# Kernel tuning notes

Measured on AMD Instinct MI355X. Metric: run time of the kernel, lower is better.

## Reference

```python
import jax, jax.numpy as jnp
import numpy as np

NUM_GROUPS = 512
GROUP_SIZE = 32
GROUP_RADIUS = 0.2
K_ORIGINAL = 5 * GROUP_SIZE  # ball_query oversampling factor from the source


def setup_inputs() -> dict:
    key = jax.random.key(0)
    k1, k2 = jax.random.split(key)
    B, N, C = 8, 16384, 4
    points = jax.random.normal(k1, (B, N, C), dtype=jnp.float32)
    # valid lengths in [N//2, N) so the lengths-masking path is exercised
    lengths = (N // 2 + jax.random.randint(k2, (B,), 0, N // 2)).astype(jnp.int32)
    return {"points": points, "lengths": lengths}


def _sample_farthest_points(xyz, lengths, K):
    # xyz: (B,N,3) float, lengths: (B,) int -> centers (B,K,3)
    B, N, _ = xyz.shape
    n_idx = jnp.arange(N)

    def per_batch(pts, length):
        valid = n_idx < length

        def step(carry, _):
            mindist, cur = carry
            d = jnp.sum((pts - pts[cur]) ** 2, axis=-1)  # (N,)
            mindist = jnp.where(valid, jnp.minimum(mindist, d), -jnp.inf)
            nxt = jnp.argmax(mindist).astype(jnp.int32)
            return (mindist, nxt), cur

        mindist0 = jnp.where(valid, jnp.inf, -jnp.inf)
        # deterministic start at index 0 (source uses random_start_point=True)
        (_, _), sel = jax.lax.scan(step, (mindist0, jnp.int32(0)), None, length=K)
        return pts[sel]

    return jax.vmap(per_batch)(xyz, lengths)


def _ball_query(centers, xyz, lengths, K, radius):
    # returns first-K (by point index, matching pytorch3d ball_query) indices
    # within radius; -1 padding. centers (B,G,3), xyz (B,N,3) -> idx (B,G,K)
    B, G, _ = centers.shape
    N = xyz.shape[1]
    d2 = jnp.sum((centers[:, :, None, :] - xyz[:, None, :, :]) ** 2, axis=-1)  # (B,G,N)
    valid = (jnp.arange(N) < lengths[:, None])[:, None, :]  # (B,1,N)
    mask = (d2 < radius * radius) & valid
    # score N-n > 0 iff in ball; top_k picks smallest indices first (in order)
    score = jnp.where(mask, N - jnp.arange(N, dtype=jnp.int32), jnp.int32(-1))
    vals, _ = jax.lax.top_k(score, K)
    return jnp.where(vals > 0, N - vals, -1)  # (B,G,K)


def _select_topk_by_energy(points, idx, K_new):
    # points (B,N,C), idx (B,G,K_orig) with -1 invalid -> (B,G,K_new)
    B, G, _ = idx.shape
    N = points.shape[1]
    invalid = idx == -1
    idxc = jnp.maximum(idx, 0)
    energies = jnp.broadcast_to(points[:, None, :, 3], (B, G, N))
    e = jnp.take_along_axis(energies, idxc, axis=2)  # (B,G,K_orig)
    e = jnp.where(invalid, -jnp.inf, e)
    top_e, top_i = jax.lax.top_k(e, K_new)
    topk_idx = jnp.take_along_axis(idx, top_i, axis=2)
    return jnp.where(top_e == -jnp.inf, -1, topk_idx)


def _masked_gather(points, idx):
    # points (B,N,C), idx (B,G,K); -1 -> gathered value 0.0 (pytorch3d semantics)
    B, G, K = idx.shape
    C = points.shape[-1]
    valid = idx >= 0
    flat = jnp.maximum(idx, 0).reshape(B, G * K)
    g = jnp.take_along_axis(points, flat[:, :, None], axis=1).reshape(B, G, K, C)
    return jnp.where(valid[..., None], g, 0.0)


def _forward(points, lengths):
    xyz = points[:, :, :3]
    centers = _sample_farthest_points(xyz, lengths, NUM_GROUPS)  # (B,G,3)
    idx = _ball_query(centers, xyz, lengths, K_ORIGINAL, GROUP_RADIUS)
    idx = _select_topk_by_energy(points, idx, GROUP_SIZE)  # (B,G,K)
    # fill_empty_indices: replace -1 with first index of the group
    first = idx[:, :, :1]
    idx = jnp.where(idx == -1, first, idx)
    groups = _masked_gather(points, idx)  # (B,G,K,C)
    groups = jnp.concatenate(
        [groups[..., :3] - centers[:, :, None, :], groups[..., 3:]], axis=-1
    )
    groups = groups / GROUP_RADIUS
    return groups, centers


def reference(points, lengths):
    return _forward(points, lengths)
```

## Files before the change

### kernel.cpp

```cpp
#include <hip/hip_runtime.h>

constexpr int B_ = 8;
constexpr int N_ = 16384;
constexpr int NG = 512;
constexpr int GS = 32;
constexpr int KORIG = 160;
constexpr int TPB = 512;
constexpr int PPT = 32;
#define R2 0.04f
#define RADIUS 0.2f

__device__ __forceinline__ unsigned f32_ord(float f) {
  unsigned u = __float_as_uint(f);
  return (u & 0x80000000u) ? ~u : (u | 0x80000000u);
}

template <int CTRL>
__device__ __forceinline__ float dpp_fmax(float v) {
  int o = __builtin_amdgcn_update_dpp(0, __float_as_int(v), CTRL, 0xF, 0xF, true);
  return fmaxf(v, __int_as_float(o));
}
__device__ __forceinline__ float wave_fmax(float v) {
  v = dpp_fmax<0xB1>(v);
  v = dpp_fmax<0x4E>(v);
  v = dpp_fmax<0x141>(v);
  v = dpp_fmax<0x140>(v);
  v = fmaxf(v, __int_as_float(__builtin_amdgcn_ds_swizzle(__float_as_int(v), 0x401F)));
  v = fmaxf(v, __shfl_xor(v, 32, 64));
  return v;
}
__device__ __forceinline__ float group8_fmax(float v) {
  v = dpp_fmax<0xB1>(v);
  v = dpp_fmax<0x4E>(v);
  v = dpp_fmax<0x141>(v);
  return v;
}

__global__ __launch_bounds__(512) void fps_kernel(const float4* __restrict__ p4,
                                                  const int* __restrict__ lengths,
                                                  float* __restrict__ centers) {
#pragma clang fp contract(off)
  const int b = blockIdx.x;
  const int t = threadIdx.x;
  const int lane = t & 63;
  const int wid = t >> 6;
  const int len = lengths[b];
  const float4* bp = p4 + (size_t)b * N_;

  __shared__ unsigned long long pub[2][8];

  float x[PPT], y[PPT], z[PPT], m[PPT];
#pragma unroll
  for (int j = 0; j < PPT; ++j) {
    const int i = t * PPT + j;
    float4 p = bp[i];
    x[j] = p.x; y[j] = p.y; z[j] = p.z;
    m[j] = (i < len) ? __builtin_inff() : -__builtin_inff();
  }

  float4 c0 = bp[0];
  float cx = c0.x, cy = c0.y, cz = c0.z;
  if (t == 0) {
    size_t o = (size_t)b * NG * 3;
    centers[o] = cx; centers[o + 1] = cy; centers[o + 2] = cz;
  }

  for (int k = 0; k < NG - 1; ++k) {
#pragma unroll
    for (int j = 0; j < PPT; ++j) {
      float dx = x[j] - cx;
      float dy = y[j] - cy;
      float dz = z[j] - cz;
      float d = dx * dx + dy * dy + dz * dz;
      m[j] = fminf(m[j], d);
    }
    float u0 = fmaxf(m[0], m[1]),   u1 = fmaxf(m[2], m[3]);
    float u2 = fmaxf(m[4], m[5]),   u3 = fmaxf(m[6], m[7]);
    float u4 = fmaxf(m[8], m[9]),   u5 = fmaxf(m[10], m[11]);
    float u6 = fmaxf(m[12], m[13]), u7 = fmaxf(m[14], m[15]);
    float u8 = fmaxf(m[16], m[17]), u9 = fmaxf(m[18], m[19]);
    float uA = fmaxf(m[20], m[21]), uB = fmaxf(m[22], m[23]);
    float uC = fmaxf(m[24], m[25]), uD = fmaxf(m[26], m[27]);
    float uE = fmaxf(m[28], m[29]), uF = fmaxf(m[30], m[31]);
    float v0 = fmaxf(u0, u1), v1 = fmaxf(u2, u3), v2 = fmaxf(u4, u5), v3 = fmaxf(u6, u7);
    float v4 = fmaxf(u8, u9), v5 = fmaxf(uA, uB), v6 = fmaxf(uC, uD), v7 = fmaxf(uE, uF);
    float w0 = fmaxf(v0, v1), w1 = fmaxf(v2, v3), w2 = fmaxf(v4, v5), w3 = fmaxf(v6, v7);
    const float sm = fmaxf(fmaxf(w0, w1), fmaxf(w2, w3));
    int bj = 31;
#pragma unroll
    for (int j = 30; j >= 0; --j) bj = (m[j] == sm) ? j : bj;

    const float wmax = wave_fmax(sm);
    const unsigned long long att = __ballot(sm == wmax);
    const int wl = __ffsll((unsigned long long)att) - 1;
    if (lane == wl) {
      pub[k & 1][wid] = ((unsigned long long)__float_as_uint(wmax) << 32) |
                        (unsigned)(t * PPT + bj);
    }
    __syncthreads();

    const unsigned long long pv = pub[k & 1][lane & 7];
    const float pw = __uint_as_float((unsigned)(pv >> 32));
    const int pi = (int)(unsigned)(pv & 0xFFFFFFFFull);
    const float4 pc = bp[pi];
    const float kmax = group8_fmax(pw);
    const unsigned long long bal = __ballot(pw == kmax);
    const int grp = lane & 56;
    const int winw = grp + (__ffsll((bal >> grp) & 0xFFull) - 1);
    cx = __shfl(pc.x, winw, 64);
    cy = __shfl(pc.y, winw, 64);
    cz = __shfl(pc.z, winw, 64);

    if (t == 0) {
      size_t o = ((size_t)b * NG + (k + 1)) * 3;
      centers[o] = cx; centers[o + 1] = cy; centers[o + 2] = cz;
    }
  }
}

__global__ __launch_bounds__(64) void group_kernel(const float4* __restrict__ p4,
                                                   const int* __restrict__ lengths,
                                                   const float* __restrict__ centers,
                                                   float4* __restrict__ outg) {
#pragma clang fp contract(off)
  const int gid = blockIdx.x;
  const int b = gid >> 9;
  const int lane = threadIdx.x;
  const int len = lengths[b];
  const float4* bp = p4 + (size_t)b * N_;
  const float cx = centers[(size_t)gid * 3 + 0];
  const float cy = centers[(size_t)gid * 3 + 1];
  const float cz = centers[(size_t)gid * 3 + 2];

  __shared__ int cand[KORIG];
  int M = 0;
  for (int cb = 0; cb < N_ && M < KORIG; cb += 256) {
#pragma unroll
    for (int q = 0; q < 4; ++q) {
      const int i = cb + q * 64 + lane;
      float4 p = bp[i];
      float dx = p.x - cx;
      float dy = p.y - cy;
      float dz = p.z - cz;
      float d2 = dx * dx + dy * dy + dz * dz;
      const bool pred = (i < len) && (d2 < R2);
      unsigned long long mb = __ballot(pred);
      if (pred) {
        int pos = M + (int)__popcll(mb & ((1ull << lane) - 1ull));
        if (pos < KORIG) cand[pos] = i;
      }
      M += (int)__popcll(mb);
    }
  }
  if (M > KORIG) M = KORIG;
  __syncthreads();

  const unsigned long long SENT = ~0ull;
  unsigned long long key0 = SENT, key1 = SENT, key2 = SENT;
  {
    int c0 = lane, c1 = lane + 64, c2 = lane + 128;
    if (c0 < M) { int i = cand[c0]; key0 = ((unsigned long long)(~f32_ord(bp[i].w)) << 32) | (unsigned)i; }
    if (c1 < M) { int i = cand[c1]; key1 = ((unsigned long long)(~f32_ord(bp[i].w)) << 32) | (unsigned)i; }
    if (c2 < M) { int i = cand[c2]; key2 = ((unsigned long long)(~f32_ord(bp[i].w)) << 32) | (unsigned)i; }
  }

  int mysel = -1;
  for (int j = 0; j < GS; ++j) {
    unsigned long long kmin = key0 < key1 ? key0 : key1;
    if (key2 < kmin) kmin = key2;
#pragma unroll
    for (int off = 32; off > 0; off >>= 1) {
      unsigned long long o = __shfl_xor(kmin, off, 64);
      if (o < kmin) kmin = o;
    }
    if (kmin == SENT) break;
    if (lane == j) mysel = (int)(unsigned)kmin;
    if (key0 == kmin) key0 = SENT;
    if (key1 == kmin) key1 = SENT;
    if (key2 == kmin) key2 = SENT;
  }

  const int first = __shfl(mysel, 0, 64);
  if (lane < GS) {
    int idx = (mysel < 0) ? first : mysel;
    float4 o;
    if (idx >= 0) {
      float4 p = bp[idx];
      o.x = (p.x - cx) / RADIUS;
      o.y = (p.y - cy) / RADIUS;
      o.z = (p.z - cz) / RADIUS;
      o.w = p.w / RADIUS;
    } else {
      o.x = (0.0f - cx) / RADIUS;
      o.y = (0.0f - cy) / RADIUS;
      o.z = (0.0f - cz) / RADIUS;
      o.w = 0.0f;
    }
    outg[(size_t)gid * GS + lane] = o;
  }
}

extern "C" void kernel_launch(void* const* d_in, const int* in_sizes, int n_in,
                              void* d_out, int out_size, void* d_ws, size_t ws_size,
                              hipStream_t stream) {
  const float4* pts = (const float4*)d_in[0];
  const int* lengths = (const int*)d_in[1];
  float* out = (float*)d_out;
  float* centers = out + (size_t)B_ * NG * GS * 4;
  float4* groups = (float4*)out;

  fps_kernel<<<B_, TPB, 0, stream>>>(pts, lengths, centers);
  group_kernel<<<B_ * NG, 64, 0, stream>>>(pts, lengths, centers, groups);
}
```

Before: 1.003 ms.

## Resolve FPS argmax in winning wave from registers instead of global reload

Result: slower. 1.204 ms (+20.1%).

```diff
diff --git a/kernel.cpp b/kernel.cpp
--- a/kernel.cpp
+++ b/kernel.cpp
@@ -36,9 +36,9 @@
   return v;
 }
 
-__global__ __launch_bounds__(512) void fps_kernel(const float4* __restrict__ p4,
-                                                  const int* __restrict__ lengths,
-                                                  float* __restrict__ centers) {
+__global__ __launch_bounds__(512, 2) void fps_kernel(const float4* __restrict__ p4,
+                                                     const int* __restrict__ lengths,
+                                                     float* __restrict__ centers) {
 #pragma clang fp contract(off)
   const int b = blockIdx.x;
   const int t = threadIdx.x;
@@ -47,7 +47,8 @@
   const int len = lengths[b];
   const float4* bp = p4 + (size_t)b * N_;
 
-  __shared__ unsigned long long pub[2][8];
+  __shared__ float pubf[8];
+  __shared__ float4 cpub;
 
   float x[PPT], y[PPT], z[PPT], m[PPT];
 #pragma unroll
@@ -86,31 +87,36 @@
     float v4 = fmaxf(u8, u9), v5 = fmaxf(uA, uB), v6 = fmaxf(uC, uD), v7 = fmaxf(uE, uF);
     float w0 = fmaxf(v0, v1), w1 = fmaxf(v2, v3), w2 = fmaxf(v4, v5), w3 = fmaxf(v6, v7);
     const float sm = fmaxf(fmaxf(w0, w1), fmaxf(w2, w3));
-    int bj = 31;
-#pragma unroll
-    for (int j = 30; j >= 0; --j) bj = (m[j] == sm) ? j : bj;
 
     const float wmax = wave_fmax(sm);
-    const unsigned long long att = __ballot(sm == wmax);
-    const int wl = __ffsll((unsigned long long)att) - 1;
-    if (lane == wl) {
-      pub[k & 1][wid] = ((unsigned long long)__float_as_uint(wmax) << 32) |
-                        (unsigned)(t * PPT + bj);
-    }
+    if (lane == 0) pubf[wid] = wmax;
     __syncthreads();
 
-    const unsigned long long pv = pub[k & 1][lane & 7];
-    const float pw = __uint_as_float((unsigned)(pv >> 32));
-    const int pi = (int)(unsigned)(pv & 0xFFFFFFFFull);
-    const float4 pc = bp[pi];
+    const float pw = pubf[lane & 7];
     const float kmax = group8_fmax(pw);
     const unsigned long long bal = __ballot(pw == kmax);
     const int grp = lane & 56;
-    const int winw = grp + (__ffsll((bal >> grp) & 0xFFull) - 1);
-    cx = __shfl(pc.x, winw, 64);
-    cy = __shfl(pc.y, winw, 64);
-    cz = __shfl(pc.z, winw, 64);
-
+    const int ww = __ffsll((bal >> grp) & 0xFFull) - 1;
+
+    if (wid == ww) {
+      float gx = x[0], gy = y[0], gz = z[0];
+      bool fnd = (m[0] == kmax);
+#pragma unroll
+      for (int j = 1; j < PPT; ++j) {
+        const bool sel = (m[j] == kmax) && !fnd;
+        gx = sel ? x[j] : gx;
+        gy = sel ? y[j] : gy;
+        gz = sel ? z[j] : gz;
+        fnd = fnd || sel;
+      }
+      const unsigned long long mb = __ballot(fnd);
+      const int wl = __ffsll(mb) - 1;
+      if (lane == wl) cpub = make_float4(gx, gy, gz, 0.0f);
+    }
+    __syncthreads();
+
+    const float4 c = cpub;
+    cx = c.x; cy = c.y; cz = c.z;
     if (t == 0) {
       size_t o = ((size_t)b * NG + (k + 1)) * 3;
       centers[o] = cx; centers[o + 1] = cy; centers[o + 2] = cz;
```
